# Kernel optimization log

Measured on AMD Instinct MI355X. Metric: run time of the kernel, lower is better.

Reference implementation:

```python
import jax, jax.numpy as jnp
import numpy as np

N_INST = 100000
N_NET = 100000
E = 1600000
H = 64
OUT = 32
L = 2


def setup_inputs() -> dict:
    key = jax.random.key(0)
    ks = jax.random.split(key, 16)
    inp = {
        "x_inst": jax.random.normal(ks[0], (N_INST, H), jnp.float32),
        "x_net": jax.random.normal(ks[1], (N_NET, H), jnp.float32),
        "edge_i2n": jax.random.randint(ks[2], (2, E), 0, N_INST, jnp.int32),
        "edge_n2i": jax.random.randint(ks[3], (2, E), 0, N_NET, jnp.int32),
        # stacked GAT params: axis0 = layer, axis1 = relation (0: inst->net, 1: net->inst)
        "W_src": jax.random.normal(ks[4], (L, 2, H, H), jnp.float32) * 0.1,
        "W_dst": jax.random.normal(ks[5], (L, 2, H, H), jnp.float32) * 0.1,
        "att_src": jax.random.normal(ks[6], (L, 2, H), jnp.float32) * 0.1,
        "att_dst": jax.random.normal(ks[7], (L, 2, H), jnp.float32) * 0.1,
        "bias_g": jax.random.normal(ks[8], (L, 2, H), jnp.float32) * 0.1,
        "lin1_w": jax.random.normal(ks[9], (H, OUT), jnp.float32) * 0.1,
        "lin1_b": jax.random.normal(ks[10], (OUT,), jnp.float32) * 0.1,
        "lin2_w": jax.random.normal(ks[11], (OUT, 1), jnp.float32) * 0.1,
        "lin2_b": jax.random.normal(ks[12], (1,), jnp.float32) * 0.1,
    }
    return inp


def _segment_softmax(scores, seg, n_seg):
    # numerically stable softmax over edges grouped by destination node
    m = jax.ops.segment_max(scores, seg, num_segments=n_seg)
    e = jnp.exp(scores - m[seg])
    s = jax.ops.segment_sum(e, seg, num_segments=n_seg)
    return e / (s[seg] + 1e-16)


def _gat_conv(x_src, x_dst, edge, Ws, Wd, a_s, a_d, b, n_dst):
    # PyG GATConv, heads=1, add_self_loops=False, eval mode (dropout inactive)
    hs = x_src @ Ws  # [Ns, H]
    hd = x_dst @ Wd  # [Nd, H]
    src, dst = edge[0], edge[1]
    score = (hs * a_s).sum(-1)[src] + (hd * a_d).sum(-1)[dst]  # [E]
    alpha = _segment_softmax(jax.nn.leaky_relu(score, 0.2), dst, n_dst)
    out = jax.ops.segment_sum(hs[src] * alpha[:, None], dst, num_segments=n_dst)
    return out + b


def reference(x_inst, x_net, edge_i2n, edge_n2i, W_src, W_dst, att_src, att_dst,
              bias_g, lin1_w, lin1_b, lin2_w, lin2_b):
    xi, xn = x_inst, x_net
    for l in range(L):
        new_net = _gat_conv(xi, xn, edge_i2n, W_src[l, 0], W_dst[l, 0],
                            att_src[l, 0], att_dst[l, 0], bias_g[l, 0], xn.shape[0])
        new_inst = _gat_conv(xn, xi, edge_n2i, W_src[l, 1], W_dst[l, 1],
                             att_src[l, 1], att_dst[l, 1], bias_g[l, 1], xi.shape[0])
        xn = jax.nn.relu(new_net)
        xi = jax.nn.relu(new_inst)
    h = jax.nn.relu(xn @ lin1_w + lin1_b)
    return h @ lin2_w + lin2_b  # [N_net, 1]
```

## Files before the change

### kernel.cpp

```cpp
#include <hip/hip_runtime.h>
#include <hip/hip_fp16.h>

#define H 64
#define BSHIFT 9
#define BUCKET 512
#define NBMAX 256
#define CHUNK 4096
#define PREF 32

__device__ __forceinline__ int bcasti(int x, int j) {
    return __builtin_amdgcn_readlane(x, j);
}
__device__ __forceinline__ float bcastf(float x, int j) {
    return __uint_as_float((unsigned)__builtin_amdgcn_readlane((int)__float_as_uint(x), j));
}

__device__ __forceinline__ float ldf(const float* p) { return *p; }
__device__ __forceinline__ float ldf(const __half* p) { return __half2float(*p); }

__global__ void wvec3_kernel(const float* __restrict__ W_dst, const float* __restrict__ att_dst,
                             float* __restrict__ v2all) {
    int b = blockIdx.x;
    int k = threadIdx.x;
    const float* Wd = W_dst + (size_t)b * H * H;
    const float* ad = att_dst + (size_t)b * H;
    float s2 = 0.f;
    for (int j = 0; j < H; ++j) s2 += Wd[k * H + j] * ad[j];
    v2all[b * H + k] = s2;
}

template <typename T>
__device__ __forceinline__ void proj_body(float* __restrict__ Wl, int blk,
                                          const T* __restrict__ x, const float* __restrict__ W,
                                          const float* __restrict__ as_, const float* __restrict__ v2d,
                                          __half* __restrict__ hs, float* __restrict__ ssrc,
                                          float* __restrict__ sdst_out, int n) {
    int t = threadIdx.x;
    for (int i = t; i < H * H; i += 256) Wl[i] = W[i];
    __syncthreads();
    int lane = t & 63;
    int w = t >> 6;
    int row0 = blk * 16 + w * 4;
    if (row0 >= n) return;
    int rem = n - row0;
    float asl = as_[lane];
    const T* xp = x + (size_t)row0 * H + lane;
    float xr0 = ldf(xp);
    float xr1 = rem > 1 ? ldf(xp + H) : 0.f;
    float xr2 = rem > 2 ? ldf(xp + 2 * H) : 0.f;
    float xr3 = rem > 3 ? ldf(xp + 3 * H) : 0.f;
    float a0 = 0.f, a1 = 0.f, a2 = 0.f, a3 = 0.f;
#pragma unroll
    for (int k = 0; k < H; ++k) {
        float wv = Wl[k * H + lane];
        a0 = fmaf(bcastf(xr0, k), wv, a0);
        a1 = fmaf(bcastf(xr1, k), wv, a1);
        a2 = fmaf(bcastf(xr2, k), wv, a2);
        a3 = fmaf(bcastf(xr3, k), wv, a3);
    }
    __half* hp = hs + (size_t)row0 * H + lane;
    hp[0] = __float2half_rn(a0);
    if (rem > 1) hp[H] = __float2half_rn(a1);
    if (rem > 2) hp[2 * H] = __float2half_rn(a2);
    if (rem > 3) hp[3 * H] = __float2half_rn(a3);
    float p0 = a0 * asl, p1 = a1 * asl, p2 = a2 * asl, p3 = a3 * asl;
#pragma unroll
    for (int off = 32; off; off >>= 1) {
        p0 += __shfl_xor(p0, off); p1 += __shfl_xor(p1, off);
        p2 += __shfl_xor(p2, off); p3 += __shfl_xor(p3, off);
    }
    if (lane == 0) {
        ssrc[row0] = p0;
        if (rem > 1) ssrc[row0 + 1] = p1;
        if (rem > 2) ssrc[row0 + 2] = p2;
        if (rem > 3) ssrc[row0 + 3] = p3;
    }
    if (sdst_out) {
        float vl = v2d[lane];
        float q0 = xr0 * vl, q1 = xr1 * vl, q2 = xr2 * vl, q3 = xr3 * vl;
#pragma unroll
        for (int off = 32; off; off >>= 1) {
            q0 += __shfl_xor(q0, off); q1 += __shfl_xor(q1, off);
            q2 += __shfl_xor(q2, off); q3 += __shfl_xor(q3, off);
        }
        if (lane == 0) {
            sdst_out[row0] = q0;
            if (rem > 1) sdst_out[row0 + 1] = q1;
            if (rem > 2) sdst_out[row0 + 2] = q2;
            if (rem > 3) sdst_out[row0 + 3] = q3;
        }
    }
}

__global__ void hist_proj_kernel(const int* __restrict__ dstA, const int* __restrict__ dstB,
                                 int* __restrict__ cntA, int* __restrict__ cntB,
                                 int ne, int nch, int nbA, int nbB,
                                 const float* __restrict__ x, const float* __restrict__ W,
                                 const float* __restrict__ as_, const float* __restrict__ v2d,
                                 __half* __restrict__ hs, float* __restrict__ ssrc,
                                 float* __restrict__ sdst_out, int n) {
    __shared__ float smem[H * H];
    int blk = blockIdx.x;
    if (blk < 2 * nch) {
        int* h = (int*)smem;
        bool second = blk >= nch;
        const int* dst = second ? dstB : dstA;
        int* cnt = second ? cntB : cntA;
        int nb = second ? nbB : nbA;
        int c = second ? blk - nch : blk;
        int beg = c * CHUNK, end = beg + CHUNK;
        if (end > ne) end = ne;
        int t = threadIdx.x;
        for (int i = t; i < NBMAX; i += 256) h[i] = 0;
        __syncthreads();
        for (int i = beg + t; i < end; i += 256) atomicAdd(&h[dst[i] >> BSHIFT], 1);
        __syncthreads();
        for (int b = t; b < nb; b += 256) cnt[(size_t)b * nch + c] = h[b];
        return;
    }
    proj_body<float>(smem, blk - 2 * nch, x, W, as_, v2d, hs, ssrc, sdst_out, n);
}

__global__ void scan_chunks(int* __restrict__ cntA, int* __restrict__ cntB,
                            int* __restrict__ totA, int* __restrict__ totB,
                            int nch, int nbA) {
    __shared__ int sm[512];
    int b = blockIdx.x;
    bool second = b >= nbA;
    int* cnt = second ? cntB : cntA;
    int* tot = second ? totB : totA;
    if (second) b -= nbA;
    int t = threadIdx.x;
    int v = t < nch ? cnt[(size_t)b * nch + t] : 0;
    sm[t] = v;
    __syncthreads();
    for (int off = 1; off < 512; off <<= 1) {
        int u = t >= off ? sm[t - off] : 0;
        __syncthreads();
        sm[t] += u;
        __syncthreads();
    }
    if (t < nch) cnt[(size_t)b * nch + t] = sm[t] - v;
    if (t == 511) tot[b] = sm[511];
}

__global__ void scan_buckets(const int* __restrict__ totA, const int* __restrict__ totB,
                             int* __restrict__ bstartA, int* __restrict__ bstartB,
                             int nbA, int nbB, int ne) {
    __shared__ int sm[256];
    const int* tot = blockIdx.x ? totB : totA;
    int* bstart = blockIdx.x ? bstartB : bstartA;
    int nb = blockIdx.x ? nbB : nbA;
    int t = threadIdx.x;
    int v = t < nb ? tot[t] : 0;
    sm[t] = v;
    __syncthreads();
    for (int off = 1; off < 256; off <<= 1) {
        int u = t >= off ? sm[t - off] : 0;
        __syncthreads();
        sm[t] += u;
        __syncthreads();
    }
    if (t < nb) bstart[t] = sm[t] - v;
    if (t == 0) bstart[nb] = ne;
}

__global__ void scatter_proj_kernel(const int* __restrict__ srcA, const int* __restrict__ dstA,
                                    const int* __restrict__ cntA, const int* __restrict__ bstartA,
                                    unsigned* __restrict__ tmpA,
                                    const int* __restrict__ srcB, const int* __restrict__ dstB,
                                    const int* __restrict__ cntB, const int* __restrict__ bstartB,
                                    unsigned* __restrict__ tmpB,
                                    int ne, int nch, int nbA, int nbB,
                                    const float* __restrict__ x, const float* __restrict__ W,
                                    const float* __restrict__ as_, const float* __restrict__ v2d,
                                    __half* __restrict__ hs, float* __restrict__ ssrc,
                                    float* __restrict__ sdst_out, int n) {
    __shared__ float smem[H * H];
    int blk = blockIdx.x;
    if (blk < 2 * nch) {
        int* cur = (int*)smem;
        bool second = blk >= nch;
        const int* src = second ? srcB : srcA;
        const int* dst = second ? dstB : dstA;
        const int* cnt = second ? cntB : cntA;
        const int* bstart = second ? bstartB : bstartA;
        unsigned* tmp = second ? tmpB : tmpA;
        int nb = second ? nbB : nbA;
        int c = second ? blk - nch : blk;
        int beg = c * CHUNK, end = beg + CHUNK;
        if (end > ne) end = ne;
        int t = threadIdx.x;
        for (int b = t; b < nb; b += 256) cur[b] = bstart[b] + cnt[(size_t)b * nch + c];
        __syncthreads();
        for (int i = beg + t; i < end; i += 256) {
            int d = dst[i];
            int pos = atomicAdd(&cur[d >> BSHIFT], 1);
            unsigned rec = ((unsigned)(d & (BUCKET - 1)) << 17) | (unsigned)src[i];
            tmp[pos] = rec;
        }
        return;
    }
    proj_body<float>(smem, blk - 2 * nch, x, W, as_, v2d, hs, ssrc, sdst_out, n);
}

__global__ void proj_half_kernel(const __half* __restrict__ x, const float* __restrict__ W,
                                 const float* __restrict__ as_,
                                 __half* __restrict__ hs, float* __restrict__ ssrc, int n) {
    __shared__ float smem[H * H];
    proj_body<__half>(smem, blockIdx.x, x, W, as_, nullptr, hs, ssrc, nullptr, n);
}

__global__ void bucket_finalize(const unsigned* __restrict__ tmpA, const int* __restrict__ bstartA,
                                int* __restrict__ rowptrA, int* __restrict__ srcsA,
                                int ndstA, int nbA,
                                const unsigned* __restrict__ tmpB, const int* __restrict__ bstartB,
                                int* __restrict__ rowptrB, int* __restrict__ srcsB,
                                int ndstB) {
    __shared__ int cnt[BUCKET];
    __shared__ int sm[BUCKET];
    __shared__ int cur[BUCKET];
    int b = blockIdx.x;
    bool second = b >= nbA;
    const unsigned* tmp = second ? tmpB : tmpA;
    const int* bstart = second ? bstartB : bstartA;
    int* rowptr = second ? rowptrB : rowptrA;
    int* srcs   = second ? srcsB : srcsA;
    int ndst    = second ? ndstB : ndstA;
    if (second) b -= nbA;

    int t = threadIdx.x;
    int base = bstart[b], endi = bstart[b + 1];
    cnt[t] = 0;
    __syncthreads();
    for (int i = base + t; i < endi; i += 512)
        atomicAdd(&cnt[tmp[i] >> 17], 1);
    __syncthreads();
    int c0 = cnt[t];
    sm[t] = c0;
    __syncthreads();
    for (int off = 1; off < 512; off <<= 1) {
        int u = t >= off ? sm[t - off] : 0;
        __syncthreads();
        sm[t] += u;
        __syncthreads();
    }
    int d0 = b << BSHIFT;
    int e = base + sm[t] - c0;
    cur[t] = e;
    if (d0 + t < ndst) rowptr[d0 + t] = e;
    if (t == 0) {
        int hi = d0 + BUCKET;
        if (hi > ndst) hi = ndst;
        rowptr[hi] = endi;
    }
    __syncthreads();
    for (int i = base + t; i < endi; i += 512) {
        unsigned rec = tmp[i];
        int pos = atomicAdd(&cur[rec >> 17], 1);
        srcs[pos] = (int)(rec & 0x1FFFFu);
    }
}

__device__ __forceinline__ float gat_aggregate(const int* __restrict__ rowptr,
                                               const int* __restrict__ srcs,
                                               const float* __restrict__ ssrc,
                                               float sdst,
                                               const __half* __restrict__ hs,
                                               const float* __restrict__ bias,
                                               int wid, int lane) {
    int beg = rowptr[wid], end = rowptr[wid + 1];
    int cnt = end - beg;
    float acc0 = 0.f, acc1 = 0.f, acc2 = 0.f, acc3 = 0.f;
    float acc4 = 0.f, acc5 = 0.f, acc6 = 0.f, acc7 = 0.f;
    float l;

    if (cnt <= 64) {
        bool valid = lane < cnt;
        int s_l = valid ? srcs[beg + lane] : 0;
        float ss = valid ? ssrc[s_l] : 0.f;

        const __half* hsl = hs + lane;
        __half hv[PREF];
#pragma unroll
        for (int k = 0; k < PREF; ++k) {
            hv[k] = hsl[(size_t)bcasti(s_l, k) * H];
        }

        float sc = ss + sdst;
        sc = sc > 0.f ? sc : 0.2f * sc;
        float ev_l = valid ? __expf(sc) : 0.f;
        float ll = ev_l;
#pragma unroll
        for (int off = 32; off; off >>= 1) ll += __shfl_xor(ll, off);
        l = ll;

#pragma unroll
        for (int k = 0; k < PREF; k += 8) {
            acc0 += bcastf(ev_l, k + 0) * __half2float(hv[k + 0]);
            acc1 += bcastf(ev_l, k + 1) * __half2float(hv[k + 1]);
            acc2 += bcastf(ev_l, k + 2) * __half2float(hv[k + 2]);
            acc3 += bcastf(ev_l, k + 3) * __half2float(hv[k + 3]);
            acc4 += bcastf(ev_l, k + 4) * __half2float(hv[k + 4]);
            acc5 += bcastf(ev_l, k + 5) * __half2float(hv[k + 5]);
            acc6 += bcastf(ev_l, k + 6) * __half2float(hv[k + 6]);
            acc7 += bcastf(ev_l, k + 7) * __half2float(hv[k + 7]);
        }
        int j = PREF;
        for (; j + 3 < cnt; j += 4) {
            acc0 += bcastf(ev_l, j + 0) * __half2float(hsl[(size_t)bcasti(s_l, j + 0) * H]);
            acc1 += bcastf(ev_l, j + 1) * __half2float(hsl[(size_t)bcasti(s_l, j + 1) * H]);
            acc2 += bcastf(ev_l, j + 2) * __half2float(hsl[(size_t)bcasti(s_l, j + 2) * H]);
            acc3 += bcastf(ev_l, j + 3) * __half2float(hsl[(size_t)bcasti(s_l, j + 3) * H]);
        }
        for (; j < cnt; ++j)
            acc0 += bcastf(ev_l, j) * __half2float(hsl[(size_t)bcasti(s_l, j) * H]);
    } else {
        const __half* hsl = hs + lane;
        float mm = -3.4e38f;
        for (int base = beg; base < end; base += 64) {
            int idx = base + lane;
            if (idx < end) {
                float sc = ssrc[srcs[idx]] + sdst;
                sc = sc > 0.f ? sc : 0.2f * sc;
                mm = fmaxf(mm, sc);
            }
        }
#pragma unroll
        for (int off = 32; off; off >>= 1) mm = fmaxf(mm, __shfl_xor(mm, off));
        float ll = 0.f;
        for (int base = beg; base < end; base += 64) {
            int idx = base + lane;
            int c2 = end - base; if (c2 > 64) c2 = 64;
            int s_l = idx < end ? srcs[idx] : 0;
            float ev_l = 0.f;
            if (idx < end) {
                float sc = ssrc[s_l] + sdst;
                sc = sc > 0.f ? sc : 0.2f * sc;
                ev_l = __expf(sc - mm);
            }
            ll += ev_l;
            int j = 0;
            for (; j + 1 < c2; j += 2) {
                acc0 += bcastf(ev_l, j) * __half2float(hsl[(size_t)bcasti(s_l, j) * H]);
                acc1 += bcastf(ev_l, j + 1) * __half2float(hsl[(size_t)bcasti(s_l, j + 1) * H]);
            }
            if (j < c2)
                acc0 += bcastf(ev_l, j) * __half2float(hsl[(size_t)bcasti(s_l, j) * H]);
        }
#pragma unroll
        for (int off = 32; off; off >>= 1) ll += __shfl_xor(ll, off);
        l = ll;
    }
    float v = ((acc0 + acc1) + (acc2 + acc3)) + ((acc4 + acc5) + (acc6 + acc7));
    v = v / (l + 1e-16f) + bias[lane];
    return v > 0.f ? v : 0.f;
}

__global__ void gat01_kernel(const int* __restrict__ rp0, const int* __restrict__ sr0,
                             const float* __restrict__ ssrc0, const float* __restrict__ sdst0,
                             const __half* __restrict__ hs0, const float* __restrict__ bias0,
                             const float* __restrict__ v2next, float* __restrict__ sdstNext, int n0,
                             const int* __restrict__ rp1, const int* __restrict__ sr1,
                             const float* __restrict__ ssrc1, const float* __restrict__ sdst1,
                             const __half* __restrict__ hs1, const float* __restrict__ bias1,
                             __half* __restrict__ out1, int n1) {
    int nblk0 = (n0 + 3) / 4;
    int lane = threadIdx.x & 63;
    if ((int)blockIdx.x < nblk0) {
        int wid = (int)((blockIdx.x * blockDim.x + threadIdx.x) >> 6);
        if (wid >= n0) return;
        float v = gat_aggregate(rp0, sr0, ssrc0, sdst0[wid], hs0, bias0, wid, lane);
        float q = v * v2next[lane];
#pragma unroll
        for (int off = 32; off; off >>= 1) q += __shfl_xor(q, off);
        if (lane == 0) sdstNext[wid] = q;
    } else {
        int wid = (int)(((blockIdx.x - nblk0) * blockDim.x + threadIdx.x) >> 6);
        if (wid >= n1) return;
        float v = gat_aggregate(rp1, sr1, ssrc1, sdst1[wid], hs1, bias1, wid, lane);
        out1[(size_t)wid * H + lane] = __float2half_rn(v);
    }
}

__global__ void gat_node_mlp_kernel(const int* __restrict__ rowptr, const int* __restrict__ srcs,
                                    const float* __restrict__ ssrc, const float* __restrict__ sdstArr,
                                    const __half* __restrict__ hs, const float* __restrict__ bias,
                                    const float* __restrict__ w1, const float* __restrict__ b1,
                                    const float* __restrict__ w2, const float* __restrict__ b2,
                                    float* __restrict__ out, int ndst) {
    __shared__ float W1[H * 32];
    __shared__ float W2[32];
    __shared__ float B1[32];
    {
        int t = threadIdx.x;
        for (int i = t; i < H * 32; i += 256) W1[i] = w1[i];
        if (t < 32) { W2[t] = w2[t]; B1[t] = b1[t]; }
        __syncthreads();
    }
    int wid = (int)((blockIdx.x * blockDim.x + threadIdx.x) >> 6);
    int lane = threadIdx.x & 63;
    if (wid >= ndst) return;
    float v = gat_aggregate(rowptr, srcs, ssrc, sdstArr[wid], hs, bias, wid, lane);

    int c = lane & 31;
    int kbase = (lane >> 5) << 5;
    float s = 0.f;
#pragma unroll
    for (int k = 0; k < 32; ++k) s += __shfl(v, kbase + k) * W1[(kbase + k) * 32 + c];
    s += __shfl_xor(s, 32);
    s += B1[c];
    s = s > 0.f ? s : 0.f;
    float q = s * W2[c];
#pragma unroll
    for (int off = 16; off; off >>= 1) q += __shfl_xor(q, off);
    if (lane == 0) out[wid] = q + b2[0];
}

extern "C" void kernel_launch(void* const* d_in, const int* in_sizes, int n_in,
                              void* d_out, int out_size, void* d_ws, size_t ws_size,
                              hipStream_t stream) {
    const float* x_inst  = (const float*)d_in[0];
    const float* x_net   = (const float*)d_in[1];
    const int*   e_i2n   = (const int*)d_in[2];
    const int*   e_n2i   = (const int*)d_in[3];
    const float* W_src   = (const float*)d_in[4];
    const float* W_dst   = (const float*)d_in[5];
    const float* att_src = (const float*)d_in[6];
    const float* att_dst = (const float*)d_in[7];
    const float* bias_g  = (const float*)d_in[8];
    const float* lin1_w  = (const float*)d_in[9];
    const float* lin1_b  = (const float*)d_in[10];
    const float* lin2_w  = (const float*)d_in[11];
    const float* lin2_b  = (const float*)d_in[12];

    const int n_inst = in_sizes[0] / H;
    const int n_net  = in_sizes[1] / H;
    const int ne     = in_sizes[2] / 2;
    const int nmax   = n_inst > n_net ? n_inst : n_net;

    const int nbA = (n_net + BUCKET - 1) >> BSHIFT;
    const int nbB = (n_inst + BUCKET - 1) >> BSHIFT;
    const int nch = (ne + CHUNK - 1) / CHUNK;

    float* ws = (float*)d_ws;
    size_t off = 0;
    auto alloc = [&](size_t nelem) {
        off = (off + 3) & ~(size_t)3;
        float* p = ws + off; off += nelem; return p;
    };
    __half* xiA    = (__half*)alloc((size_t)n_inst * H / 2);
    __half* hs0    = (__half*)alloc((size_t)nmax * H / 2);
    __half* hs1    = (__half*)alloc((size_t)nmax * H / 2);
    __half* hs2    = (__half*)alloc((size_t)nmax * H / 2);
    float* ssrc0   = alloc(nmax);
    float* ssrc1   = alloc(nmax);
    float* ssrc2   = alloc(nmax);
    float* sdstA   = alloc(nmax);
    float* sdstB   = alloc(nmax);
    float* sdstC   = alloc(nmax);
    int*   rp_i2n  = (int*)alloc(nmax + 1);
    int*   sr_i2n  = (int*)alloc(ne);
    int*   rp_n2i  = (int*)alloc(nmax + 1);
    int*   sr_n2i  = (int*)alloc(ne);
    unsigned* tmpA = (unsigned*)alloc(ne);
    unsigned* tmpB = (unsigned*)alloc(ne);
    int*   cntA    = (int*)alloc((size_t)NBMAX * nch);
    int*   cntB    = (int*)alloc((size_t)NBMAX * nch);
    int*   totA    = (int*)alloc(NBMAX);
    int*   totB    = (int*)alloc(NBMAX);
    int*   bstartA = (int*)alloc(NBMAX + 1);
    int*   bstartB = (int*)alloc(NBMAX + 1);
    float* v2all   = alloc(3 * H);
    (void)ws_size;

    const int* dstA = e_i2n + ne;
    const int* dstB = e_n2i + ne;

    wvec3_kernel<<<3, 64, 0, stream>>>(W_dst, att_dst, v2all);

    {
        int grid = 2 * nch + (n_inst + 15) / 16;
        hist_proj_kernel<<<grid, 256, 0, stream>>>(dstA, dstB, cntA, cntB, ne, nch, nbA, nbB,
                                                   x_inst, W_src + 0 * H * H, att_src + 0 * H,
                                                   v2all + 1 * H, hs0, ssrc0, sdstB, n_inst);
    }
    scan_chunks<<<nbA + nbB, 512, 0, stream>>>(cntA, cntB, totA, totB, nch, nbA);
    scan_buckets<<<2, 256, 0, stream>>>(totA, totB, bstartA, bstartB, nbA, nbB, ne);
    {
        int grid = 2 * nch + (n_net + 15) / 16;
        scatter_proj_kernel<<<grid, 256, 0, stream>>>(e_i2n, dstA, cntA, bstartA, tmpA,
                                                      e_n2i, dstB, cntB, bstartB, tmpB,
                                                      ne, nch, nbA, nbB,
                                                      x_net, W_src + 1 * H * H, att_src + 1 * H,
                                                      v2all + 0 * H, hs1, ssrc1, sdstA, n_net);
    }
    bucket_finalize<<<nbA + nbB, 512, 0, stream>>>(tmpA, bstartA, rp_i2n, sr_i2n, n_net, nbA,
                                                   tmpB, bstartB, rp_n2i, sr_n2i, n_inst);

    {
        int grid = (n_net + 3) / 4 + (n_inst + 3) / 4;
        gat01_kernel<<<grid, 256, 0, stream>>>(rp_i2n, sr_i2n, ssrc0, sdstA, hs0, bias_g + 0 * H,
                                               v2all + 2 * H, sdstC, n_net,
                                               rp_n2i, sr_n2i, ssrc1, sdstB, hs1, bias_g + 1 * H,
                                               xiA, n_inst);
    }
    proj_half_kernel<<<(n_inst + 15) / 16, 256, 0, stream>>>(xiA, W_src + 2 * H * H,
                                                             att_src + 2 * H, hs2, ssrc2, n_inst);
    gat_node_mlp_kernel<<<(n_net + 3) / 4, 256, 0, stream>>>(rp_i2n, sr_i2n, ssrc2, sdstC,
                                                             hs2, bias_g + 2 * H,
                                                             lin1_w, lin1_b, lin2_w, lin2_b,
                                                             (float*)d_out, n_net);
}
```

Before: 329.2 us.

## Regroup layer-0 GAT kernels to overlap net aggregation with layer-1 projection

Splits the fused layer-0 aggregation kernel so the net->inst aggregation runs first on its own. The inst->net aggregation then shares one launch with the layer-1 source projection of the new instance features, so the projection's blocks run alongside the aggregation instead of in a separate launch. It also adds a 16-edge prefetch specialisation for nodes with small degree. With an average degree of 16, that path should issue fewer wasted gathers. The cost is a different kernel mix with a larger shared-memory footprint in the combined kernel, which may reduce occupancy for the aggregation blocks.

```diff
diff --git a/kernel.cpp b/kernel.cpp
--- a/kernel.cpp
+++ b/kernel.cpp
@@ -6,7 +6,6 @@
 #define BUCKET 512
 #define NBMAX 256
 #define CHUNK 4096
-#define PREF 32
 
 __device__ __forceinline__ int bcasti(int x, int j) {
     return __builtin_amdgcn_readlane(x, j);
@@ -204,13 +203,6 @@
     proj_body<float>(smem, blk - 2 * nch, x, W, as_, v2d, hs, ssrc, sdst_out, n);
 }
 
-__global__ void proj_half_kernel(const __half* __restrict__ x, const float* __restrict__ W,
-                                 const float* __restrict__ as_,
-                                 __half* __restrict__ hs, float* __restrict__ ssrc, int n) {
-    __shared__ float smem[H * H];
-    proj_body<__half>(smem, blockIdx.x, x, W, as_, nullptr, hs, ssrc, nullptr, n);
-}
-
 __global__ void bucket_finalize(const unsigned* __restrict__ tmpA, const int* __restrict__ bstartA,
                                 int* __restrict__ rowptrA, int* __restrict__ srcsA,
                                 int ndstA, int nbA,
@@ -262,6 +254,58 @@
     }
 }
 
+template <int P>
+__device__ __forceinline__ float gat_fast(const int* __restrict__ srcs, int beg, int cnt,
+                                          const float* __restrict__ ssrc, float sdst,
+                                          const __half* __restrict__ hs,
+                                          const float* __restrict__ bias, int lane) {
+    bool valid = lane < cnt;
+    int s_l = valid ? srcs[beg + lane] : 0;
+    float ss = valid ? ssrc[s_l] : 0.f;
+
+    const __half* hsl = hs + lane;
+    __half hv[P];
+#pragma unroll
+    for (int k = 0; k < P; ++k) {
+        hv[k] = hsl[(size_t)bcasti(s_l, k) * H];
+    }
+
+    float sc = ss + sdst;
+    sc = sc > 0.f ? sc : 0.2f * sc;
+    float ev_l = valid ? __expf(sc) : 0.f;
+    float ll = ev_l;
+#pragma unroll
+    for (int off = 32; off; off >>= 1) ll += __shfl_xor(ll, off);
+
+    float acc0 = 0.f, acc1 = 0.f, acc2 = 0.f, acc3 = 0.f;
+    float acc4 = 0.f, acc5 = 0.f, acc6 = 0.f, acc7 = 0.f;
+#pragma unroll
+    for (int k = 0; k < P; k += 8) {
+        acc0 += bcastf(ev_l, k + 0) * __half2float(hv[k + 0]);
+        acc1 += bcastf(ev_l, k + 1) * __half2float(hv[k + 1]);
+        acc2 += bcastf(ev_l, k + 2) * __half2float(hv[k + 2]);
+        acc3 += bcastf(ev_l, k + 3) * __half2float(hv[k + 3]);
+        acc4 += bcastf(ev_l, k + 4) * __half2float(hv[k + 4]);
+        acc5 += bcastf(ev_l, k + 5) * __half2float(hv[k + 5]);
+        acc6 += bcastf(ev_l, k + 6) * __half2float(hv[k + 6]);
+        acc7 += bcastf(ev_l, k + 7) * __half2float(hv[k + 7]);
+    }
+    if constexpr (P == 32) {
+        int j = P;
+        for (; j + 3 < cnt; j += 4) {
+            acc0 += bcastf(ev_l, j + 0) * __half2float(hsl[(size_t)bcasti(s_l, j + 0) * H]);
+            acc1 += bcastf(ev_l, j + 1) * __half2float(hsl[(size_t)bcasti(s_l, j + 1) * H]);
+            acc2 += bcastf(ev_l, j + 2) * __half2float(hsl[(size_t)bcasti(s_l, j + 2) * H]);
+            acc3 += bcastf(ev_l, j + 3) * __half2float(hsl[(size_t)bcasti(s_l, j + 3) * H]);
+        }
+        for (; j < cnt; ++j)
+            acc0 += bcastf(ev_l, j) * __half2float(hsl[(size_t)bcasti(s_l, j) * H]);
+    }
+    float v = ((acc0 + acc1) + (acc2 + acc3)) + ((acc4 + acc5) + (acc6 + acc7));
+    v = v / (ll + 1e-16f) + bias[lane];
+    return v > 0.f ? v : 0.f;
+}
+
 __device__ __forceinline__ float gat_aggregate(const int* __restrict__ rowptr,
                                                const int* __restrict__ srcs,
                                                const float* __restrict__ ssrc,
@@ -271,116 +315,80 @@
                                                int wid, int lane) {
     int beg = rowptr[wid], end = rowptr[wid + 1];
     int cnt = end - beg;
-    float acc0 = 0.f, acc1 = 0.f, acc2 = 0.f, acc3 = 0.f;
-    float acc4 = 0.f, acc5 = 0.f, acc6 = 0.f, acc7 = 0.f;
-    float l;
-
-    if (cnt <= 64) {
-        bool valid = lane < cnt;
-        int s_l = valid ? srcs[beg + lane] : 0;
-        float ss = valid ? ssrc[s_l] : 0.f;
-
-        const __half* hsl = hs + lane;
-        __half hv[PREF];
-#pragma unroll
-        for (int k = 0; k < PREF; ++k) {
-            hv[k] = hsl[(size_t)bcasti(s_l, k) * H];
-        }
-
-        float sc = ss + sdst;
-        sc = sc > 0.f ? sc : 0.2f * sc;
-        float ev_l = valid ? __expf(sc) : 0.f;
-        float ll = ev_l;
-#pragma unroll
-        for (int off = 32; off; off >>= 1) ll += __shfl_xor(ll, off);
-        l = ll;
-
-#pragma unroll
-        for (int k = 0; k < PREF; k += 8) {
-            acc0 += bcastf(ev_l, k + 0) * __half2float(hv[k + 0]);
-            acc1 += bcastf(ev_l, k + 1) * __half2float(hv[k + 1]);
-            acc2 += bcastf(ev_l, k + 2) * __half2float(hv[k + 2]);
-            acc3 += bcastf(ev_l, k + 3) * __half2float(hv[k + 3]);
-            acc4 += bcastf(ev_l, k + 4) * __half2float(hv[k + 4]);
-            acc5 += bcastf(ev_l, k + 5) * __half2float(hv[k + 5]);
-            acc6 += bcastf(ev_l, k + 6) * __half2float(hv[k + 6]);
-            acc7 += bcastf(ev_l, k + 7) * __half2float(hv[k + 7]);
-        }
-        int j = PREF;
-        for (; j + 3 < cnt; j += 4) {
-            acc0 += bcastf(ev_l, j + 0) * __half2float(hsl[(size_t)bcasti(s_l, j + 0) * H]);
+    if (cnt <= 16) return gat_fast<16>(srcs, beg, cnt, ssrc, sdst, hs, bias, lane);
+    if (cnt <= 64) return gat_fast<32>(srcs, beg, cnt, ssrc, sdst, hs, bias, lane);
+
+    const __half* hsl = hs + lane;
+    float acc0 = 0.f, acc1 = 0.f;
+    float mm = -3.4e38f;
+    for (int base = beg; base < end; base += 64) {
+        int idx = base + lane;
+        if (idx < end) {
+            float sc = ssrc[srcs[idx]] + sdst;
+            sc = sc > 0.f ? sc : 0.2f * sc;
+            mm = fmaxf(mm, sc);
+        }
+    }
+#pragma unroll
+    for (int off = 32; off; off >>= 1) mm = fmaxf(mm, __shfl_xor(mm, off));
+    float ll = 0.f;
+    for (int base = beg; base < end; base += 64) {
+        int idx = base + lane;
+        int c2 = end - base; if (c2 > 64) c2 = 64;
+        int s_l = idx < end ? srcs[idx] : 0;
+        float ev_l = 0.f;
+        if (idx < end) {
+            float sc = ssrc[s_l] + sdst;
+            sc = sc > 0.f ? sc : 0.2f * sc;
+            ev_l = __expf(sc - mm);
+        }
+        ll += ev_l;
+        int j = 0;
+        for (; j + 1 < c2; j += 2) {
+            acc0 += bcastf(ev_l, j) * __half2float(hsl[(size_t)bcasti(s_l, j) * H]);
             acc1 += bcastf(ev_l, j + 1) * __half2float(hsl[(size_t)bcasti(s_l, j + 1) * H]);
-            acc2 += bcastf(ev_l, j + 2) * __half2float(hsl[(size_t)bcasti(s_l, j + 2) * H]);
-            acc3 += bcastf(ev_l, j + 3) * __half2float(hsl[(size_t)bcasti(s_l, j + 3) * H]);
-        }
-        for (; j < cnt; ++j)
+        }
+        if (j < c2)
             acc0 += bcastf(ev_l, j) * __half2float(hsl[(size_t)bcasti(s_l, j) * H]);
-    } else {
-        const __half* hsl = hs + lane;
-        float mm = -3.4e38f;
-        for (int base = beg; base < end; base += 64) {
-            int idx = base + lane;
-            if (idx < end) {
-                float sc = ssrc[srcs[idx]] + sdst;
-                sc = sc > 0.f ? sc : 0.2f * sc;
-                mm = fmaxf(mm, sc);
-            }
-        }
-#pragma unroll
-        for (int off = 32; off; off >>= 1) mm = fmaxf(mm, __shfl_xor(mm, off));
-        float ll = 0.f;
-        for (int base = beg; base < end; base += 64) {
-            int idx = base + lane;
-            int c2 = end - base; if (c2 > 64) c2 = 64;
-            int s_l = idx < end ? srcs[idx] : 0;
-            float ev_l = 0.f;
-            if (idx < end) {
-                float sc = ssrc[s_l] + sdst;
-                sc = sc > 0.f ? sc : 0.2f * sc;
-                ev_l = __expf(sc - mm);
-            }
-            ll += ev_l;
-            int j = 0;
-            for (; j + 1 < c2; j += 2) {
-                acc0 += bcastf(ev_l, j) * __half2float(hsl[(size_t)bcasti(s_l, j) * H]);
-                acc1 += bcastf(ev_l, j + 1) * __half2float(hsl[(size_t)bcasti(s_l, j + 1) * H]);
-            }
-            if (j < c2)
-                acc0 += bcastf(ev_l, j) * __half2float(hsl[(size_t)bcasti(s_l, j) * H]);
-        }
-#pragma unroll
-        for (int off = 32; off; off >>= 1) ll += __shfl_xor(ll, off);
-        l = ll;
-    }
-    float v = ((acc0 + acc1) + (acc2 + acc3)) + ((acc4 + acc5) + (acc6 + acc7));
-    v = v / (l + 1e-16f) + bias[lane];
+    }
+#pragma unroll
+    for (int off = 32; off; off >>= 1) ll += __shfl_xor(ll, off);
+    float v = (acc0 + acc1) / (ll + 1e-16f) + bias[lane];
     return v > 0.f ? v : 0.f;
 }
 
-__global__ void gat01_kernel(const int* __restrict__ rp0, const int* __restrict__ sr0,
-                             const float* __restrict__ ssrc0, const float* __restrict__ sdst0,
-                             const __half* __restrict__ hs0, const float* __restrict__ bias0,
-                             const float* __restrict__ v2next, float* __restrict__ sdstNext, int n0,
-                             const int* __restrict__ rp1, const int* __restrict__ sr1,
-                             const float* __restrict__ ssrc1, const float* __restrict__ sdst1,
-                             const __half* __restrict__ hs1, const float* __restrict__ bias1,
-                             __half* __restrict__ out1, int n1) {
+__global__ void gat1_kernel(const int* __restrict__ rp1, const int* __restrict__ sr1,
+                            const float* __restrict__ ssrc1, const float* __restrict__ sdst1,
+                            const __half* __restrict__ hs1, const float* __restrict__ bias1,
+                            __half* __restrict__ out1, int n1) {
+    int wid = (int)((blockIdx.x * blockDim.x + threadIdx.x) >> 6);
+    int lane = threadIdx.x & 63;
+    if (wid >= n1) return;
+    float v = gat_aggregate(rp1, sr1, ssrc1, sdst1[wid], hs1, bias1, wid, lane);
+    out1[(size_t)wid * H + lane] = __float2half_rn(v);
+}
+
+__global__ void gat0_proj_kernel(const int* __restrict__ rp0, const int* __restrict__ sr0,
+                                 const float* __restrict__ ssrc0, const float* __restrict__ sdst0,
+                                 const __half* __restrict__ hs0, const float* __restrict__ bias0,
+                                 const float* __restrict__ v2next, float* __restrict__ sdstNext, int n0,
+                                 const __half* __restrict__ xiA, const float* __restrict__ Wsrc2,
+                                 const float* __restrict__ as2,
+                                 __half* __restrict__ hs2, float* __restrict__ ssrc2, int n1) {
+    __shared__ float smem[H * H];
     int nblk0 = (n0 + 3) / 4;
-    int lane = threadIdx.x & 63;
     if ((int)blockIdx.x < nblk0) {
         int wid = (int)((blockIdx.x * blockDim.x + threadIdx.x) >> 6);
+        int lane = threadIdx.x & 63;
         if (wid >= n0) return;
         float v = gat_aggregate(rp0, sr0, ssrc0, sdst0[wid], hs0, bias0, wid, lane);
         float q = v * v2next[lane];
 #pragma unroll
         for (int off = 32; off; off >>= 1) q += __shfl_xor(q, off);
         if (lane == 0) sdstNext[wid] = q;
-    } else {
-        int wid = (int)(((blockIdx.x - nblk0) * blockDim.x + threadIdx.x) >> 6);
-        if (wid >= n1) return;
-        float v = gat_aggregate(rp1, sr1, ssrc1, sdst1[wid], hs1, bias1, wid, lane);
-        out1[(size_t)wid * H + lane] = __float2half_rn(v);
-    }
+        return;
+    }
+    proj_body<__half>(smem, blockIdx.x - nblk0, xiA, Wsrc2, as2, nullptr, hs2, ssrc2, nullptr, n1);
 }
 
 __global__ void gat_node_mlp_kernel(const int* __restrict__ rowptr, const int* __restrict__ srcs,
@@ -498,15 +506,15 @@
     bucket_finalize<<<nbA + nbB, 512, 0, stream>>>(tmpA, bstartA, rp_i2n, sr_i2n, n_net, nbA,
                                                    tmpB, bstartB, rp_n2i, sr_n2i, n_inst);
 
+    gat1_kernel<<<(n_inst + 3) / 4, 256, 0, stream>>>(rp_n2i, sr_n2i, ssrc1, sdstB,
+                                                      hs1, bias_g + 1 * H, xiA, n_inst);
     {
-        int grid = (n_net + 3) / 4 + (n_inst + 3) / 4;
-        gat01_kernel<<<grid, 256, 0, stream>>>(rp_i2n, sr_i2n, ssrc0, sdstA, hs0, bias_g + 0 * H,
-                                               v2all + 2 * H, sdstC, n_net,
-                                               rp_n2i, sr_n2i, ssrc1, sdstB, hs1, bias_g + 1 * H,
-                                               xiA, n_inst);
-    }
-    proj_half_kernel<<<(n_inst + 15) / 16, 256, 0, stream>>>(xiA, W_src + 2 * H * H,
-                                                             att_src + 2 * H, hs2, ssrc2, n_inst);
+        int grid = (n_net + 3) / 4 + (n_inst + 15) / 16;
+        gat0_proj_kernel<<<grid, 256, 0, stream>>>(rp_i2n, sr_i2n, ssrc0, sdstA, hs0,
+                                                   bias_g + 0 * H, v2all + 2 * H, sdstC, n_net,
+                                                   xiA, W_src + 2 * H * H, att_src + 2 * H,
+                                                   hs2, ssrc2, n_inst);
+    }
     gat_node_mlp_kernel<<<(n_net + 3) / 4, 256, 0, stream>>>(rp_i2n, sr_i2n, ssrc2, sdstC,
                                                              hs2, bias_g + 2 * H,
                                                              lin1_w, lin1_b, lin2_w, lin2_b,
```

After: 330.9 us. Within noise of the previous version (+0.5%).
